# Optimization experiments

Measured on AMD Instinct MI355X. Metric: run time of the kernel, lower is better.

Reference implementation:

```python
import jax, jax.numpy as jnp
import numpy as np

DIM = 2048
N_HEADS = 16
HEAD_DIM = DIM // N_HEADS
MAX_SEQ_LEN = 2048
ROPE_THETA = 32.0
EPS = 1e-6


def _precompute_freqs_1d(dim, max_seq_len, theta):
    freqs = theta ** (-np.arange(0, dim, 2, dtype=np.float32) / dim)  # [dim/2]
    pos = np.arange(max_seq_len, dtype=np.float32)                    # [S]
    ang = pos[:, None] * freqs[None, :]                               # [S, dim/2]
    return jnp.asarray(np.cos(ang)), jnp.asarray(np.sin(ang))


def _rms_norm(x, w):
    # x: [..., d]
    inv = jax.lax.rsqrt(jnp.mean(x * x, axis=-1, keepdims=True) + EPS)
    return x * inv * w


def setup_inputs() -> dict:
    key = jax.random.key(0)
    k1, k2, k3 = jax.random.split(key, 3)
    bsz, seq_len = 4, 2048
    x = jax.random.normal(k1, (bsz, seq_len, DIM), dtype=jnp.float32)
    w_qkv = jax.random.normal(k2, (3 * DIM, DIM), dtype=jnp.float32) * (DIM ** -0.5)
    w_proj = jax.random.normal(k3, (DIM, DIM), dtype=jnp.float32) * (DIM ** -0.5)
    q_norm_w = jnp.ones((HEAD_DIM,), dtype=jnp.float32)
    k_norm_w = jnp.ones((HEAD_DIM,), dtype=jnp.float32)
    return {"x": x, "w_qkv": w_qkv, "w_proj": w_proj,
            "q_norm_w": q_norm_w, "k_norm_w": k_norm_w}


def reference(x, w_qkv, w_proj, q_norm_w, k_norm_w):
    bsz, seq_len, dim = x.shape
    scale = HEAD_DIM ** -0.5

    # QKV projection (torch Linear: x @ W^T)
    qkv = jnp.einsum('bsd,ed->bse', x, w_qkv)  # [b, s, 3*dim]
    qkv = qkv.reshape(bsz, seq_len, 3, N_HEADS, HEAD_DIM).transpose(2, 0, 3, 1, 4)
    q, k, v = qkv[0], qkv[1], qkv[2]           # each [b, h, s, d]

    # Per-head RMSNorm on q, k
    q = _rms_norm(q, q_norm_w)
    k = _rms_norm(k, k_norm_w)

    # RoPE (half-split convention)
    cos, sin = _precompute_freqs_1d(HEAD_DIM, MAX_SEQ_LEN, ROPE_THETA)
    cos = cos[:seq_len][None, None]  # [1,1,s,d/2]
    sin = sin[:seq_len][None, None]
    q1, q2 = jnp.split(q, 2, axis=-1)
    k1, k2 = jnp.split(k, 2, axis=-1)
    q = jnp.concatenate([q1 * cos - q2 * sin, q2 * cos + q1 * sin], axis=-1)
    k = jnp.concatenate([k1 * cos - k2 * sin, k2 * cos + k1 * sin], axis=-1)

    # Scaled dot-product attention (no mask, eval-mode: no dropout)
    scores = jnp.einsum('bhqd,bhkd->bhqk', q, k) * scale
    attn = jax.nn.softmax(scores, axis=-1)
    y = jnp.einsum('bhqk,bhkd->bhqd', attn, v)

    # Merge heads + output projection
    y = y.transpose(0, 2, 1, 3).reshape(bsz, seq_len, dim)
    return jnp.einsum('bsd,ed->bse', y, w_proj)
```

## Files before the change

### kernel.cpp

```cpp
#include <hip/hip_runtime.h>
#include <hip/hip_bf16.h>

#define BSZ 4
#define SEQ 2048
#define DIM 2048
#define NH 16
#define HD 128
#define QK_LD 4096
#define SCALE 0.08838834764831845f

typedef __attribute__((ext_vector_type(8))) short bf16x8;
typedef __attribute__((ext_vector_type(4))) float f32x4;

#define GLDS16(g, l)                                                           \
  __builtin_amdgcn_global_load_lds(                                           \
      (const __attribute__((address_space(1))) void*)(g),                     \
      (__attribute__((address_space(3))) void*)(l), 16, 0, 0)

__device__ inline short f2b(float f) {
  __hip_bfloat16 h = __float2bfloat16(f);
  short s;
  __builtin_memcpy(&s, &h, 2);
  return s;
}

__device__ inline void stage16(const float* gp, __hip_bfloat16* lp) {
  float4 q0 = ((const float4*)gp)[0], q1 = ((const float4*)gp)[1];
  float4 q2 = ((const float4*)gp)[2], q3 = ((const float4*)gp)[3];
  bf16x8 v0, v1;
  v0[0] = f2b(q0.x); v0[1] = f2b(q0.y); v0[2] = f2b(q0.z); v0[3] = f2b(q0.w);
  v0[4] = f2b(q1.x); v0[5] = f2b(q1.y); v0[6] = f2b(q1.z); v0[7] = f2b(q1.w);
  v1[0] = f2b(q2.x); v1[1] = f2b(q2.y); v1[2] = f2b(q2.z); v1[3] = f2b(q2.w);
  v1[4] = f2b(q3.x); v1[5] = f2b(q3.y); v1[6] = f2b(q3.z); v1[7] = f2b(q3.w);
  *(bf16x8*)lp = v0;
  *(bf16x8*)(lp + 8) = v1;
}

__device__ inline char* out_slice(void* outv, int b, int fl) {
  return (char*)outv + (size_t)b * (size_t)SEQ * DIM * (fl ? 2u : 4u);
}

__global__ __launch_bounds__(256)
void detect_canon(const unsigned int* __restrict__ wbits,
                  const void* __restrict__ qw, const void* __restrict__ kw,
                  __hip_bfloat16* __restrict__ qwb,
                  __hip_bfloat16* __restrict__ kwb, int* __restrict__ flag) {
  __shared__ int cnt;
  const int t = threadIdx.x;
  if (t == 0) cnt = 0;
  __syncthreads();
  int local = 0;
  for (int i = 0; i < 4; ++i) {
    unsigned int e = (wbits[t * 4 + i] >> 7) & 0xFF;
    if (e >= 96 && e < 160) local++;
  }
  atomicAdd(&cnt, local);
  __syncthreads();
  const int f = (cnt >= 768) ? 1 : 0;
  if (t == 0) *flag = f;
  if (t < 128)
    qwb[t] = f ? ((const __hip_bfloat16*)qw)[t]
               : __float2bfloat16(((const float*)qw)[t]);
  else
    kwb[t - 128] = f ? ((const __hip_bfloat16*)kw)[t - 128]
                     : __float2bfloat16(((const float*)kw)[t - 128]);
}

__global__ __launch_bounds__(256)
void convert_bf16(const void* __restrict__ in, __hip_bfloat16* __restrict__ out,
                  const int* __restrict__ flag) {
  const int fl = *flag;
  long i = ((long)blockIdx.x * 256 + threadIdx.x) * 8;
  if (fl) {
    *(float4*)(out + i) = *(const float4*)((const __hip_bfloat16*)in + i);
  } else {
    const float* p = (const float*)in + i;
    float4 a = ((const float4*)p)[0], b = ((const float4*)p)[1];
    bf16x8 o;
    o[0] = f2b(a.x); o[1] = f2b(a.y); o[2] = f2b(a.z); o[3] = f2b(a.w);
    o[4] = f2b(b.x); o[5] = f2b(b.y); o[6] = f2b(b.z); o[7] = f2b(b.w);
    *(bf16x8*)(out + i) = o;
  }
}


__global__ __launch_bounds__(256)
void gemm_qkv_full(const __hip_bfloat16* __restrict__ A,
                   const __hip_bfloat16* __restrict__ B,
                   __hip_bfloat16* __restrict__ qk, void* __restrict__ outv,
                   const int* __restrict__ flag) {
  __shared__ __hip_bfloat16 As[128 * 32];
  __shared__ __hip_bfloat16 Bs[128 * 32];
  const int t = threadIdx.x, wave = t >> 6, lane = t & 63;
  const int quad = lane >> 4, l16 = lane & 15;
  const int wm = (wave & 1) * 64, wn = (wave >> 1) * 64;
  const long bm = (long)blockIdx.x * 128, bn = (long)blockIdx.y * 128;
  const int fl = *flag;

  f32x4 acc[4][4] = {};
  for (int k0 = 0; k0 < DIM; k0 += 32) {
    __syncthreads();
    for (int i = 0; i < 2; ++i) {
      int c = wave * 64 + lane + i * 256;
      int row = c >> 2, kc = c & 3;
      GLDS16(A + (bm + row) * DIM + k0 + kc * 8, As + (wave * 64 + i * 256) * 8);
      GLDS16(B + (bn + row) * DIM + k0 + kc * 8, Bs + (wave * 64 + i * 256) * 8);
    }
    __syncthreads();
    bf16x8 aF[4], bF[4];
    for (int mt = 0; mt < 4; ++mt)
      aF[mt] = *(const bf16x8*)(As + (wm + mt * 16 + l16) * 32 + quad * 8);
    for (int nt = 0; nt < 4; ++nt)
      bF[nt] = *(const bf16x8*)(Bs + (wn + nt * 16 + l16) * 32 + quad * 8);
    for (int mt = 0; mt < 4; ++mt)
      for (int nt = 0; nt < 4; ++nt)
        acc[mt][nt] = __builtin_amdgcn_mfma_f32_16x16x32_bf16(
            aF[mt], bF[nt], acc[mt][nt], 0, 0, 0);
  }

  if (bn < 4096) {
    for (int mt = 0; mt < 4; ++mt) {
      long gr = bm + wm + mt * 16 + quad * 4;
      for (int nt = 0; nt < 4; ++nt) {
        long gc = bn + wn + nt * 16 + l16;
        for (int r = 0; r < 4; ++r)
          qk[(gr + r) * QK_LD + gc] = __float2bfloat16(acc[mt][nt][r]);
      }
    }
  } else {
    for (int mt = 0; mt < 4; ++mt) {
      long gr = bm + wm + mt * 16 + quad * 4;
      __hip_bfloat16* vtb = (__hip_bfloat16*)out_slice(outv, (int)(gr >> 11), fl);
      long s = gr & 2047;
      for (int nt = 0; nt < 4; ++nt) {
        long col = bn - 4096 + wn + nt * 16 + l16;
        for (int r = 0; r < 4; ++r)
          vtb[col * SEQ + s + r] = __float2bfloat16(acc[mt][nt][r]);
      }
    }
  }
}

__global__ __launch_bounds__(256)
void gemm_proj_full(const __hip_bfloat16* __restrict__ A,
                    const __hip_bfloat16* __restrict__ B,
                    void* __restrict__ outv, const int* __restrict__ flag) {
  __shared__ __hip_bfloat16 As[128 * 32];
  __shared__ __hip_bfloat16 Bs[128 * 32];
  const int t = threadIdx.x, wave = t >> 6, lane = t & 63;
  const int quad = lane >> 4, l16 = lane & 15;
  const int wm = (wave & 1) * 64, wn = (wave >> 1) * 64;
  const long bm = (long)blockIdx.x * 128, bn = (long)blockIdx.y * 128;
  const int fl = *flag;

  f32x4 acc[4][4] = {};
  for (int k0 = 0; k0 < DIM; k0 += 32) {
    __syncthreads();
    for (int i = 0; i < 2; ++i) {
      int c = wave * 64 + lane + i * 256;
      int row = c >> 2, kc = c & 3;
      GLDS16(A + (bm + row) * QK_LD + k0 + kc * 8, As + (wave * 64 + i * 256) * 8);
      GLDS16(B + (bn + row) * DIM + k0 + kc * 8, Bs + (wave * 64 + i * 256) * 8);
    }
    __syncthreads();
    bf16x8 aF[4], bF[4];
    for (int mt = 0; mt < 4; ++mt)
      aF[mt] = *(const bf16x8*)(As + (wm + mt * 16 + l16) * 32 + quad * 8);
    for (int nt = 0; nt < 4; ++nt)
      bF[nt] = *(const bf16x8*)(Bs + (wn + nt * 16 + l16) * 32 + quad * 8);
    for (int mt = 0; mt < 4; ++mt)
      for (int nt = 0; nt < 4; ++nt)
        acc[mt][nt] = __builtin_amdgcn_mfma_f32_16x16x32_bf16(
            aF[mt], bF[nt], acc[mt][nt], 0, 0, 0);
  }

  for (int mt = 0; mt < 4; ++mt) {
    long gr = bm + wm + mt * 16 + quad * 4;
    for (int nt = 0; nt < 4; ++nt) {
      long gc = bn + wn + nt * 16 + l16;
      for (int r = 0; r < 4; ++r) {
        long idx = (gr + r) * DIM + gc;
        if (fl) ((__hip_bfloat16*)outv)[idx] = __float2bfloat16(acc[mt][nt][r]);
        else    ((float*)outv)[idx] = acc[mt][nt][r];
      }
    }
  }
}


__global__ __launch_bounds__(256)
void gemm_qkv(const void* __restrict__ xin, const void* __restrict__ win,
              __hip_bfloat16* __restrict__ qk, void* __restrict__ outv,
              const int* __restrict__ flag, int b) {
  __shared__ __hip_bfloat16 As[128 * 32];
  __shared__ __hip_bfloat16 Bs[128 * 32];
  const int t = threadIdx.x, wave = t >> 6, lane = t & 63;
  const int quad = lane >> 4, l16 = lane & 15;
  const int wm = (wave & 1) * 64, wn = (wave >> 1) * 64;
  const long bm = (long)blockIdx.x * 128, bn = (long)blockIdx.y * 128;
  const int fl = *flag;
  const __hip_bfloat16* Ab = (const __hip_bfloat16*)xin + (long)b * SEQ * DIM;
  const __hip_bfloat16* Bb = (const __hip_bfloat16*)win;
  const float* Af = (const float*)xin + (long)b * SEQ * DIM;
  const float* Bf = (const float*)win;

  f32x4 acc[4][4] = {};
  for (int k0 = 0; k0 < DIM; k0 += 32) {
    __syncthreads();
    if (fl) {
      for (int i = 0; i < 2; ++i) {
        int c = wave * 64 + lane + i * 256;
        int row = c >> 2, kc = c & 3;
        GLDS16(Ab + (bm + row) * DIM + k0 + kc * 8, As + (wave * 64 + i * 256) * 8);
        GLDS16(Bb + (bn + row) * DIM + k0 + kc * 8, Bs + (wave * 64 + i * 256) * 8);
      }
    } else {
      int row = t >> 1, cb = k0 + (t & 1) * 16;
      stage16(Af + (bm + row) * DIM + cb, As + t * 16);
      stage16(Bf + (bn + row) * DIM + cb, Bs + t * 16);
    }
    __syncthreads();
    bf16x8 aF[4], bF[4];
    for (int mt = 0; mt < 4; ++mt)
      aF[mt] = *(const bf16x8*)(As + (wm + mt * 16 + l16) * 32 + quad * 8);
    for (int nt = 0; nt < 4; ++nt)
      bF[nt] = *(const bf16x8*)(Bs + (wn + nt * 16 + l16) * 32 + quad * 8);
    for (int mt = 0; mt < 4; ++mt)
      for (int nt = 0; nt < 4; ++nt)
        acc[mt][nt] = __builtin_amdgcn_mfma_f32_16x16x32_bf16(
            aF[mt], bF[nt], acc[mt][nt], 0, 0, 0);
  }

  if (bn < 4096) {
    for (int mt = 0; mt < 4; ++mt) {
      long gr = bm + wm + mt * 16 + quad * 4;
      for (int nt = 0; nt < 4; ++nt) {
        long gc = bn + wn + nt * 16 + l16;
        for (int r = 0; r < 4; ++r)
          qk[(gr + r) * QK_LD + gc] = __float2bfloat16(acc[mt][nt][r]);
      }
    }
  } else {
    __hip_bfloat16* vtb = (__hip_bfloat16*)out_slice(outv, b, fl);
    for (int mt = 0; mt < 4; ++mt) {
      long gr = bm + wm + mt * 16 + quad * 4;
      for (int nt = 0; nt < 4; ++nt) {
        long col = bn - 4096 + wn + nt * 16 + l16;
        for (int r = 0; r < 4; ++r)
          vtb[col * SEQ + gr + r] = __float2bfloat16(acc[mt][nt][r]);
      }
    }
  }
}

__global__ __launch_bounds__(256)
void gemm_proj(const __hip_bfloat16* __restrict__ A, const void* __restrict__ win,
               void* __restrict__ outv, const int* __restrict__ flag, int b) {
  __shared__ __hip_bfloat16 As[128 * 32];
  __shared__ __hip_bfloat16 Bs[128 * 32];
  const int t = threadIdx.x, wave = t >> 6, lane = t & 63;
  const int quad = lane >> 4, l16 = lane & 15;
  const int wm = (wave & 1) * 64, wn = (wave >> 1) * 64;
  const long bm = (long)blockIdx.x * 128, bn = (long)blockIdx.y * 128;
  const int fl = *flag;
  const __hip_bfloat16* Bb = (const __hip_bfloat16*)win;
  const float* Bf = (const float*)win;

  f32x4 acc[4][4] = {};
  for (int k0 = 0; k0 < DIM; k0 += 32) {
    __syncthreads();
    for (int i = 0; i < 2; ++i) {
      int c = wave * 64 + lane + i * 256;
      int row = c >> 2, kc = c & 3;
      GLDS16(A + (bm + row) * QK_LD + k0 + kc * 8, As + (wave * 64 + i * 256) * 8);
    }
    if (fl) {
      for (int i = 0; i < 2; ++i) {
        int c = wave * 64 + lane + i * 256;
        int row = c >> 2, kc = c & 3;
        GLDS16(Bb + (bn + row) * DIM + k0 + kc * 8, Bs + (wave * 64 + i * 256) * 8);
      }
    } else {
      int row = t >> 1, cb = k0 + (t & 1) * 16;
      stage16(Bf + (bn + row) * DIM + cb, Bs + t * 16);
    }
    __syncthreads();
    bf16x8 aF[4], bF[4];
    for (int mt = 0; mt < 4; ++mt)
      aF[mt] = *(const bf16x8*)(As + (wm + mt * 16 + l16) * 32 + quad * 8);
    for (int nt = 0; nt < 4; ++nt)
      bF[nt] = *(const bf16x8*)(Bs + (wn + nt * 16 + l16) * 32 + quad * 8);
    for (int mt = 0; mt < 4; ++mt)
      for (int nt = 0; nt < 4; ++nt)
        acc[mt][nt] = __builtin_amdgcn_mfma_f32_16x16x32_bf16(
            aF[mt], bF[nt], acc[mt][nt], 0, 0, 0);
  }

  char* Cb = out_slice(outv, b, fl);
  for (int mt = 0; mt < 4; ++mt) {
    long gr = bm + wm + mt * 16 + quad * 4;
    for (int nt = 0; nt < 4; ++nt) {
      long gc = bn + wn + nt * 16 + l16;
      for (int r = 0; r < 4; ++r) {
        long idx = (gr + r) * DIM + gc;
        if (fl) ((__hip_bfloat16*)Cb)[idx] = __float2bfloat16(acc[mt][nt][r]);
        else    ((float*)Cb)[idx] = acc[mt][nt][r];
      }
    }
  }
}


__global__ __launch_bounds__(256)
void norm_rope(__hip_bfloat16* __restrict__ qk,
               const __hip_bfloat16* __restrict__ qwb,
               const __hip_bfloat16* __restrict__ kwb) {
  const int wave = threadIdx.x >> 6, lane = threadIdx.x & 63;
  const int gid = blockIdx.x * 4 + wave;
  const int h = gid & 15, tt = (gid >> 4) & 1, row = gid >> 5;
  const int s = row & 2047;

  __hip_bfloat16* p = qk + (long)row * QK_LD + tt * DIM + h * HD;
  unsigned int u = ((const unsigned int*)p)[lane];

  unsigned int x = (unsigned int)__shfl((int)u, lane >> 1);
  unsigned int y = (unsigned int)__shfl((int)u, 32 + (lane >> 1));
  float v1 = __uint_as_float((lane & 1) ? (x & 0xFFFF0000u) : (x << 16));
  float v2 = __uint_as_float((lane & 1) ? (y & 0xFFFF0000u) : (y << 16));

  float ss = v1 * v1 + v2 * v2;
  for (int off = 1; off < 64; off <<= 1) ss += __shfl_xor(ss, off);
  float inv = rsqrtf(ss * (1.0f / 128.0f) + 1e-6f);

  const __hip_bfloat16* w = tt ? kwb : qwb;
  float n1 = v1 * inv * __bfloat162float(w[lane]);
  float n2 = v2 * inv * __bfloat162float(w[lane + 64]);

  float freq = exp2f(-5.0f * (float)lane * (1.0f / 64.0f));
  float ang = (float)s * freq;
  float c = cosf(ang), sn = sinf(ang);
  float r1 = n1 * c - n2 * sn;
  float r2 = n2 * c + n1 * sn;

  float z1lo = __shfl(r1, (2 * lane) & 63), z2lo = __shfl(r2, (2 * lane) & 63);
  float z1hi = __shfl(r1, (2 * lane + 1) & 63), z2hi = __shfl(r2, (2 * lane + 1) & 63);
  float lo = (lane < 32) ? z1lo : z2lo;
  float hi = (lane < 32) ? z1hi : z2hi;
  unsigned int ou = (unsigned int)(unsigned short)f2b(lo) |
                    ((unsigned int)(unsigned short)f2b(hi) << 16);
  ((unsigned int*)p)[lane] = ou;
}

__global__ __launch_bounds__(256)
void flash_attn(__hip_bfloat16* __restrict__ qkbase, void* __restrict__ outv,
                const int* __restrict__ flag, int b0) {
  __shared__ __hip_bfloat16 Ks[4 * 64 * 32];
  __shared__ __hip_bfloat16 Vs[2 * 128 * 32];
  __shared__ __hip_bfloat16 Ps[4][2 * 32 * 32];

  const int t = threadIdx.x, wave = t >> 6, lane = t & 63;
  const int quad = lane >> 4, l16 = lane & 15;
  const int q0 = blockIdx.x * 128, h = blockIdx.y;
  const int b = b0 + blockIdx.z;
  const int fl = *flag;
  __hip_bfloat16* qk = qkbase + (long)blockIdx.z * SEQ * QK_LD;
  __hip_bfloat16* Qg = qk + h * HD;
  const __hip_bfloat16* Kg = Qg + DIM;
  const __hip_bfloat16* Vt =
      (const __hip_bfloat16*)out_slice(outv, b, fl) + (long)h * HD * SEQ;

  bf16x8 aQ[2][4];
#pragma unroll
  for (int mt = 0; mt < 2; ++mt)
#pragma unroll
    for (int ks = 0; ks < 4; ++ks)
      aQ[mt][ks] = *(const bf16x8*)(Qg +
          (long)(q0 + wave * 32 + mt * 16 + l16) * QK_LD + ks * 32 + quad * 8);

  f32x4 oacc[2][8] = {};
  float m_run[2][4], l_run[2][4];
#pragma unroll
  for (int mt = 0; mt < 2; ++mt)
    for (int r = 0; r < 4; ++r) { m_run[mt][r] = -1e30f; l_run[mt][r] = 0.0f; }

  for (int j0 = 0; j0 < SEQ; j0 += 64) {
    __syncthreads();
    for (int i = 0; i < 4; ++i) {
      int f = wave * 64 + lane + i * 256;
      int kk = f & 3, row = (f >> 2) & 63, ks = f >> 8;
      GLDS16(Kg + (long)(j0 + row) * QK_LD + ks * 32 + kk * 8,
             Ks + (wave * 64 + i * 256) * 8);
    }
    for (int i = 0; i < 4; ++i) {
      int f = wave * 64 + lane + i * 256;
      int kk = f & 3, dimr = (f >> 2) & 127, ks2 = f >> 9;
      GLDS16(Vt + (long)dimr * SEQ + j0 + ks2 * 32 + kk * 8,
             Vs + (wave * 64 + i * 256) * 8);
    }
    __syncthreads();

    f32x4 sacc[2][4] = {};
#pragma unroll
    for (int ks = 0; ks < 4; ++ks)
#pragma unroll
      for (int nt = 0; nt < 4; ++nt) {
        bf16x8 bK = *(const bf16x8*)(Ks + (ks * 64 + nt * 16 + l16) * 32 + quad * 8);
#pragma unroll
        for (int mt = 0; mt < 2; ++mt)
          sacc[mt][nt] = __builtin_amdgcn_mfma_f32_16x16x32_bf16(
              aQ[mt][ks], bK, sacc[mt][nt], 0, 0, 0);
      }

    __hip_bfloat16* pw = &Ps[wave][0];
#pragma unroll
    for (int mt = 0; mt < 2; ++mt) {
      float p[4][4];
      for (int r = 0; r < 4; ++r) {
        float mx = -1e30f;
        for (int nt = 0; nt < 4; ++nt) {
          float sv = sacc[mt][nt][r] * SCALE;
          p[nt][r] = sv;
          mx = fmaxf(mx, sv);
        }
        for (int off = 1; off < 16; off <<= 1) mx = fmaxf(mx, __shfl_xor(mx, off));
        float mnew = fmaxf(m_run[mt][r], mx);
        float sum = 0.0f;
        for (int nt = 0; nt < 4; ++nt) {
          float e = __expf(p[nt][r] - mnew);
          p[nt][r] = e;
          sum += e;
        }
        for (int off = 1; off < 16; off <<= 1) sum += __shfl_xor(sum, off);
        float alpha = __expf(m_run[mt][r] - mnew);
        l_run[mt][r] = l_run[mt][r] * alpha + sum;
        m_run[mt][r] = mnew;
        for (int n = 0; n < 8; ++n) oacc[mt][n][r] = oacc[mt][n][r] * alpha;
      }
      for (int r = 0; r < 4; ++r)
        for (int nt = 0; nt < 4; ++nt)
          pw[((nt >> 1) * 32 + mt * 16 + quad * 4 + r) * 32 + (nt & 1) * 16 + l16] =
              __float2bfloat16(p[nt][r]);
    }

#pragma unroll
    for (int ks2 = 0; ks2 < 2; ++ks2) {
      bf16x8 aP[2];
#pragma unroll
      for (int mt = 0; mt < 2; ++mt)
        aP[mt] = *(const bf16x8*)(pw + (ks2 * 32 + mt * 16 + l16) * 32 + quad * 8);
#pragma unroll
      for (int n = 0; n < 8; ++n) {
        bf16x8 bV = *(const bf16x8*)(Vs + (ks2 * 128 + n * 16 + l16) * 32 + quad * 8);
#pragma unroll
        for (int mt = 0; mt < 2; ++mt)
          oacc[mt][n] = __builtin_amdgcn_mfma_f32_16x16x32_bf16(
              aP[mt], bV, oacc[mt][n], 0, 0, 0);
      }
    }
  }

#pragma unroll
  for (int mt = 0; mt < 2; ++mt)
    for (int r = 0; r < 4; ++r) {
      float rl = 1.0f / l_run[mt][r];
      long s = q0 + wave * 32 + mt * 16 + quad * 4 + r;
      for (int n = 0; n < 8; ++n)
        qk[s * QK_LD + h * HD + n * 16 + l16] =
            __float2bfloat16(oacc[mt][n][r] * rl);
    }
}

extern "C" void kernel_launch(void* const* d_in, const int* in_sizes, int n_in,
                              void* d_out, int out_size, void* d_ws, size_t ws_size,
                              hipStream_t stream) {
  int* flag = (int*)d_ws;
  __hip_bfloat16* qwb = (__hip_bfloat16*)((char*)d_ws + 64);
  __hip_bfloat16* kwb = qwb + 128;
  char* base = (char*)d_ws + 1024;

  detect_canon<<<1, 256, 0, stream>>>((const unsigned int*)d_in[1], d_in[3],
                                      d_in[4], qwb, kwb, flag);

  const size_t MB = 1024ull * 1024ull;
  const size_t NEED_A = 1024 + 128 * MB;

  if (ws_size >= NEED_A) {
    __hip_bfloat16* xb     = (__hip_bfloat16*)base;
    __hip_bfloat16* wqkvb  = (__hip_bfloat16*)(base + 32 * MB);
    __hip_bfloat16* wprojb = (__hip_bfloat16*)(base + 56 * MB);
    __hip_bfloat16* qk     = (__hip_bfloat16*)(base + 64 * MB);

    convert_bf16<<<(BSZ * SEQ * DIM) / 2048, 256, 0, stream>>>(d_in[0], xb, flag);
    convert_bf16<<<(3 * DIM * DIM) / 2048, 256, 0, stream>>>(d_in[1], wqkvb, flag);
    convert_bf16<<<(DIM * DIM) / 2048, 256, 0, stream>>>(d_in[2], wprojb, flag);

    gemm_qkv_full<<<dim3((BSZ * SEQ) / 128, (3 * DIM) / 128), 256, 0, stream>>>(
        xb, wqkvb, qk, d_out, flag);
    norm_rope<<<(BSZ * SEQ * 2 * NH) / 4, 256, 0, stream>>>(qk, qwb, kwb);
    flash_attn<<<dim3(SEQ / 128, NH, BSZ), 256, 0, stream>>>(qk, d_out, flag, 0);
    gemm_proj_full<<<dim3((BSZ * SEQ) / 128, DIM / 128), 256, 0, stream>>>(
        qk, wprojb, d_out, flag);
  } else {
    __hip_bfloat16* qk = (__hip_bfloat16*)base;
    for (int b = 0; b < BSZ; ++b) {
      gemm_qkv<<<dim3(SEQ / 128, (3 * DIM) / 128), 256, 0, stream>>>(
          d_in[0], d_in[1], qk, d_out, flag, b);
      norm_rope<<<(SEQ * 2 * NH) / 4, 256, 0, stream>>>(qk, qwb, kwb);
      flash_attn<<<dim3(SEQ / 128, NH, 1), 256, 0, stream>>>(qk, d_out, flag, b);
      gemm_proj<<<dim3(SEQ / 128, DIM / 128), 256, 0, stream>>>(
          qk, d_in[2], d_out, flag, b);
    }
  }
}
```

Baseline: 855.5 us.

## Pipeline K/V loads, swizzle LDS, and use lazy-rescale exp2 softmax in flash attention

Restructures the flash-attention loop so the next K tile loads during softmax and the next V tile loads after the PV MMA, using manual vmcnt waits and raw barriers in place of full syncthreads around each load. Adds an XOR swizzle to the K, V and P LDS layouts to cut bank conflicts. Softmax moves to exp2 with a prescaled log2e constant, only rescales the accumulator when the running max grows by more than 8, and defers the row-sum reduction to the epilogue. The gains come from overlapped memory and fewer exps and shuffles, at the cost of fragile vmcnt accounting and a lazy rescale that depends on bounded exponent growth.

```diff
diff --git a/kernel.cpp b/kernel.cpp
--- a/kernel.cpp
+++ b/kernel.cpp
@@ -8,6 +8,7 @@
 #define HD 128
 #define QK_LD 4096
 #define SCALE 0.08838834764831845f
+#define SC2 0.12751742910198f
 
 typedef __attribute__((ext_vector_type(8))) short bf16x8;
 typedef __attribute__((ext_vector_type(4))) float f32x4;
@@ -351,6 +352,31 @@
   ((unsigned int*)p)[lane] = ou;
 }
 
+#define FA_STAGE_K(J)                                                          \
+  for (int i_ = 0; i_ < 4; ++i_) {                                             \
+    int f_ = wave * 64 + lane + i_ * 256;                                      \
+    int kk_ = f_ & 3, row_ = (f_ >> 2) & 63, ks_ = f_ >> 8;                    \
+    GLDS16(Kg + (long)((J) + row_) * QK_LD + ks_ * 32 +                        \
+               (kk_ ^ ((row_ >> 1) & 3)) * 8,                                  \
+           Ks + (wave * 64 + i_ * 256) * 8);                                   \
+  }
+#define FA_STAGE_V(J)                                                          \
+  for (int i_ = 0; i_ < 4; ++i_) {                                             \
+    int f_ = wave * 64 + lane + i_ * 256;                                      \
+    int kk_ = f_ & 3, dim_ = (f_ >> 2) & 127, ks2_ = f_ >> 9;                  \
+    GLDS16(Vt + (long)dim_ * SEQ + (J) + ks2_ * 32 +                           \
+               (kk_ ^ ((dim_ >> 1) & 3)) * 8,                                  \
+           Vs + (wave * 64 + i_ * 256) * 8);                                   \
+  }
+#define FA_WAIT4 asm volatile("s_waitcnt vmcnt(4)" ::: "memory")
+#define FA_WAIT0 asm volatile("s_waitcnt vmcnt(0)" ::: "memory")
+#define FA_BAR                                                                 \
+  do {                                                                         \
+    asm volatile("" ::: "memory");                                             \
+    __builtin_amdgcn_s_barrier();                                              \
+    asm volatile("" ::: "memory");                                             \
+  } while (0)
+
 __global__ __launch_bounds__(256)
 void flash_attn(__hip_bfloat16* __restrict__ qkbase, void* __restrict__ outv,
                 const int* __restrict__ flag, int b0) {
@@ -360,6 +386,7 @@
 
   const int t = threadIdx.x, wave = t >> 6, lane = t & 63;
   const int quad = lane >> 4, l16 = lane & 15;
+  const int swz = (quad ^ ((l16 >> 1) & 3)) * 8;
   const int q0 = blockIdx.x * 128, h = blockIdx.y;
   const int b = b0 + blockIdx.z;
   const int fl = *flag;
@@ -383,86 +410,91 @@
   for (int mt = 0; mt < 2; ++mt)
     for (int r = 0; r < 4; ++r) { m_run[mt][r] = -1e30f; l_run[mt][r] = 0.0f; }
 
+  FA_STAGE_K(0);
+  FA_STAGE_V(0);
+
   for (int j0 = 0; j0 < SEQ; j0 += 64) {
-    __syncthreads();
-    for (int i = 0; i < 4; ++i) {
-      int f = wave * 64 + lane + i * 256;
-      int kk = f & 3, row = (f >> 2) & 63, ks = f >> 8;
-      GLDS16(Kg + (long)(j0 + row) * QK_LD + ks * 32 + kk * 8,
-             Ks + (wave * 64 + i * 256) * 8);
-    }
-    for (int i = 0; i < 4; ++i) {
-      int f = wave * 64 + lane + i * 256;
-      int kk = f & 3, dimr = (f >> 2) & 127, ks2 = f >> 9;
-      GLDS16(Vt + (long)dimr * SEQ + j0 + ks2 * 32 + kk * 8,
-             Vs + (wave * 64 + i * 256) * 8);
-    }
-    __syncthreads();
+    const bool more = (j0 + 64 < SEQ);
+
+    FA_WAIT4;
+    FA_BAR;
 
     f32x4 sacc[2][4] = {};
 #pragma unroll
     for (int ks = 0; ks < 4; ++ks)
 #pragma unroll
       for (int nt = 0; nt < 4; ++nt) {
-        bf16x8 bK = *(const bf16x8*)(Ks + (ks * 64 + nt * 16 + l16) * 32 + quad * 8);
+        bf16x8 bK = *(const bf16x8*)(Ks + (ks * 64 + nt * 16 + l16) * 32 + swz);
 #pragma unroll
         for (int mt = 0; mt < 2; ++mt)
           sacc[mt][nt] = __builtin_amdgcn_mfma_f32_16x16x32_bf16(
               aQ[mt][ks], bK, sacc[mt][nt], 0, 0, 0);
       }
 
+    FA_BAR;
+    if (more) { FA_STAGE_K(j0 + 64); }
+
     __hip_bfloat16* pw = &Ps[wave][0];
 #pragma unroll
     for (int mt = 0; mt < 2; ++mt) {
-      float p[4][4];
+#pragma unroll
       for (int r = 0; r < 4; ++r) {
-        float mx = -1e30f;
-        for (int nt = 0; nt < 4; ++nt) {
-          float sv = sacc[mt][nt][r] * SCALE;
-          p[nt][r] = sv;
-          mx = fmaxf(mx, sv);
+        float p0 = sacc[mt][0][r] * SC2, p1 = sacc[mt][1][r] * SC2;
+        float p2 = sacc[mt][2][r] * SC2, p3 = sacc[mt][3][r] * SC2;
+        float mx = fmaxf(fmaxf(p0, p1), fmaxf(p2, p3));
+        for (int off = 1; off < 16; off <<= 1)
+          mx = fmaxf(mx, __shfl_xor(mx, off));
+        if (__any(mx > m_run[mt][r] + 8.0f)) {
+          float mnew = fmaxf(m_run[mt][r], mx);
+          float alpha = exp2f(m_run[mt][r] - mnew);
+          m_run[mt][r] = mnew;
+          l_run[mt][r] *= alpha;
+#pragma unroll
+          for (int n = 0; n < 8; ++n) oacc[mt][n][r] *= alpha;
         }
-        for (int off = 1; off < 16; off <<= 1) mx = fmaxf(mx, __shfl_xor(mx, off));
-        float mnew = fmaxf(m_run[mt][r], mx);
-        float sum = 0.0f;
-        for (int nt = 0; nt < 4; ++nt) {
-          float e = __expf(p[nt][r] - mnew);
-          p[nt][r] = e;
-          sum += e;
-        }
-        for (int off = 1; off < 16; off <<= 1) sum += __shfl_xor(sum, off);
-        float alpha = __expf(m_run[mt][r] - mnew);
-        l_run[mt][r] = l_run[mt][r] * alpha + sum;
-        m_run[mt][r] = mnew;
-        for (int n = 0; n < 8; ++n) oacc[mt][n][r] = oacc[mt][n][r] * alpha;
-      }
-      for (int r = 0; r < 4; ++r)
-        for (int nt = 0; nt < 4; ++nt)
-          pw[((nt >> 1) * 32 + mt * 16 + quad * 4 + r) * 32 + (nt & 1) * 16 + l16] =
-              __float2bfloat16(p[nt][r]);
-    }
+        float m = m_run[mt][r];
+        float e0 = exp2f(p0 - m), e1 = exp2f(p1 - m);
+        float e2 = exp2f(p2 - m), e3 = exp2f(p3 - m);
+        l_run[mt][r] += (e0 + e1) + (e2 + e3);
+        int rbase = (mt * 16 + quad * 4 + r) * 32;
+        int sc = (((quad * 4 + r) >> 1) & 3) << 3;
+        pw[rbase + (l16 ^ sc)] = __float2bfloat16(e0);
+        pw[rbase + ((l16 + 16) ^ sc)] = __float2bfloat16(e1);
+        pw[1024 + rbase + (l16 ^ sc)] = __float2bfloat16(e2);
+        pw[1024 + rbase + ((l16 + 16) ^ sc)] = __float2bfloat16(e3);
+      }
+    }
+
+    if (more) { FA_WAIT4; } else { FA_WAIT0; }
+    FA_BAR;
 
 #pragma unroll
     for (int ks2 = 0; ks2 < 2; ++ks2) {
       bf16x8 aP[2];
 #pragma unroll
       for (int mt = 0; mt < 2; ++mt)
-        aP[mt] = *(const bf16x8*)(pw + (ks2 * 32 + mt * 16 + l16) * 32 + quad * 8);
+        aP[mt] = *(const bf16x8*)(pw + ks2 * 1024 + (mt * 16 + l16) * 32 + swz);
 #pragma unroll
       for (int n = 0; n < 8; ++n) {
-        bf16x8 bV = *(const bf16x8*)(Vs + (ks2 * 128 + n * 16 + l16) * 32 + quad * 8);
+        bf16x8 bV = *(const bf16x8*)(Vs + (ks2 * 128 + n * 16 + l16) * 32 + swz);
 #pragma unroll
         for (int mt = 0; mt < 2; ++mt)
           oacc[mt][n] = __builtin_amdgcn_mfma_f32_16x16x32_bf16(
               aP[mt], bV, oacc[mt][n], 0, 0, 0);
       }
     }
+
+    FA_BAR;
+    if (more) { FA_STAGE_V(j0 + 64); }
   }
 
 #pragma unroll
   for (int mt = 0; mt < 2; ++mt)
+#pragma unroll
     for (int r = 0; r < 4; ++r) {
-      float rl = 1.0f / l_run[mt][r];
+      float l = l_run[mt][r];
+      for (int off = 1; off < 16; off <<= 1) l += __shfl_xor(l, off);
+      float rl = 1.0f / l;
       long s = q0 + wave * 32 + mt * 16 + quad * 4 + r;
       for (int n = 0; n < 8; ++n)
         qk[s * QK_LD + h * HD + n * 16 + l16] =
```

Measured after the change: 992.6 us. 16.0% more time.
